# Kernel tuning notes

Measured on AMD Instinct MI355X. Metric: run time of the kernel, lower is better.

## Reference

```python
import jax, jax.numpy as jnp
import numpy as np

EPS = 1e-5


def conv3x3(x, w, b):
    # x [B,C,H,W], w [O,C,3,3], stride 1, pad 1
    y = jax.lax.conv_general_dilated(x, w, (1, 1), ((1, 1), (1, 1)),
                                     dimension_numbers=('NCHW', 'OIHW', 'NCHW'))
    return y + b[None, :, None, None]


def bilinear_gather(x, py, px):
    # x [B,C,H,W]; sampling locations py,px [B,K,H,W] -> [B,C,K,H,W]
    # Zero padding outside the image (matches deform_conv CUDA semantics:
    # out-of-bound corner values contribute 0).
    B, C, H, W = x.shape
    K = py.shape[1]
    x_flat = x.reshape(B, C, H * W)
    y0 = jnp.floor(py)
    x0 = jnp.floor(px)
    out = jnp.zeros((B, C, K, H, W), x.dtype)
    for dy in (0.0, 1.0):
        for dx in (0.0, 1.0):
            yi = y0 + dy
            xi = x0 + dx
            wgt = (1.0 - jnp.abs(py - yi)) * (1.0 - jnp.abs(px - xi))  # [B,K,H,W]
            valid = (yi >= 0) & (yi <= H - 1) & (xi >= 0) & (xi <= W - 1)
            idx = (jnp.clip(yi, 0, H - 1).astype(jnp.int32) * W
                   + jnp.clip(xi, 0, W - 1).astype(jnp.int32)).reshape(B, -1)
            vals = jax.vmap(lambda xf, i: xf[:, i])(x_flat, idx)  # [B,C,K*H*W]
            out = out + (wgt * valid)[:, None] * vals.reshape(B, C, K, H, W)
    return out


def setup_inputs() -> dict:
    key = jax.random.key(0)
    k1, k2, k3 = jax.random.split(key, 3)
    B, C, O, H, W = 4, 64, 64, 128, 128
    x = jax.random.normal(k1, (B, C, H, W), jnp.float32)
    # offset predictor: small init so predicted offsets are modest (realistic)
    off_w = 0.01 * jax.random.normal(k2, (18, C, 3, 3), jnp.float32)
    off_b = jnp.zeros((18,), jnp.float32)
    dc_w = jax.random.normal(k3, (O, C, 3, 3), jnp.float32) / np.sqrt(C * 9)
    dc_b = jnp.zeros((O,), jnp.float32)
    gamma = jnp.ones((O,), jnp.float32)
    beta = jnp.zeros((O,), jnp.float32)
    return {"x": x, "off_w": off_w, "off_b": off_b, "dc_w": dc_w,
            "dc_b": dc_b, "gamma": gamma, "beta": beta}


def reference(x, off_w, off_b, dc_w, dc_b, gamma, beta):
    B, C, H, W = x.shape
    O = dc_w.shape[0]
    K = 9  # 3x3 kernel
    offset = conv3x3(x, off_w, off_b)              # [B,18,H,W]
    off = offset.reshape(B, K, 2, H, W)            # (dy,dx) per kernel tap, row-major
    dyo, dxo = off[:, :, 0], off[:, :, 1]          # [B,K,H,W]
    k = (jnp.arange(3) - 1).astype(x.dtype)        # kernel taps {-1,0,1}
    kgy = jnp.repeat(k, 3)                         # [9] row-major y offsets
    kgx = jnp.tile(k, 3)                           # [9] row-major x offsets
    hh = jnp.arange(H, dtype=x.dtype)
    ww = jnp.arange(W, dtype=x.dtype)
    # stride 1, pad 1: base point = out_pos - 1 + tap; pad is folded into kgy/kgx
    py = hh[None, None, :, None] + kgy[None, :, None, None] + dyo
    px = ww[None, None, None, :] + kgx[None, :, None, None] + dxo
    sampled = bilinear_gather(x, py, px)           # [B,C,K,H,W]
    y = jnp.einsum('ock,bckhw->bohw', dc_w.reshape(O, C, K), sampled)
    y = y + dc_b[None, :, None, None]
    # BatchNorm2d (training mode: biased batch statistics)
    mu = y.mean(axis=(0, 2, 3), keepdims=True)
    var = y.var(axis=(0, 2, 3), keepdims=True)
    yn = (y - mu) * jax.lax.rsqrt(var + EPS)
    return jax.nn.relu(yn * gamma[None, :, None, None] + beta[None, :, None, None])
```

## Files before the change

### kernel.cpp

```cpp
#include <hip/hip_runtime.h>

#define HH 128
#define WW 128
#define HWSZ (HH * WW)
#define CC 64
#define OO 64
#define BB 4
#define NOFF 18
#define KK 576

#define WS_BG     0
#define WS_BGO    18432
#define WS_YBUF   27776
#define WS_PART   2125952

typedef __attribute__((ext_vector_type(8))) short short8;
typedef __attribute__((ext_vector_type(4))) int int4v;
typedef __attribute__((ext_vector_type(2))) unsigned int uint2v;
typedef __attribute__((ext_vector_type(4))) float f32x4;

__device__ inline unsigned bf16rne(float f) {
  unsigned u = __float_as_uint(f);
  u += 0x7fff + ((u >> 16) & 1);
  return u >> 16;
}

__device__ inline float bf16lo(unsigned u) { return __uint_as_float(u << 16); }
__device__ inline float bf16hi(unsigned u) { return __uint_as_float(u & 0xffff0000u); }

__global__ __launch_bounds__(256) void prep_kernel(
    const float* __restrict__ x, const float* __restrict__ off_w,
    const float* __restrict__ dc_w, unsigned int* __restrict__ xTu,
    int* __restrict__ Bg, int* __restrict__ Bgo) {
  int bid = blockIdx.x;
  if (bid < BB * HH * 2) {
    __shared__ float T[CC][64 + 1];
    int b = bid >> 8, rem = bid & 255;
    int h = rem >> 1, wh = (rem & 1) * 64;
    const float* xp = x + (size_t)b * CC * HWSZ + h * WW + wh;
    int j = threadIdx.x;
#pragma unroll
    for (int i = 0; i < 4; ++i) {
      int l = i * 256 + j;
      int c = l >> 4, w4 = l & 15;
      float4 v = *(const float4*)(xp + (size_t)c * HWSZ + w4 * 4);
      T[c][w4 * 4 + 0] = v.x;
      T[c][w4 * 4 + 1] = v.y;
      T[c][w4 * 4 + 2] = v.z;
      T[c][w4 * 4 + 3] = v.w;
    }
    __syncthreads();
    int c2 = threadIdx.x & 31, wq = threadIdx.x >> 5;
    unsigned int* op = xTu + ((size_t)(b * HH + h) * WW + wh) * 32;
#pragma unroll 8
    for (int i = 0; i < 8; ++i) {
      int w = i * 8 + wq;
      unsigned pk = bf16rne(T[2 * c2][w]) | (bf16rne(T[2 * c2 + 1][w]) << 16);
      op[w * 32 + c2] = pk;
    }
  } else {
    int pb = bid - BB * HH * 2;
    int tid = pb * 256 + threadIdx.x;
    int stride = 64 * 256;
    for (int i = tid; i < 72 * 64 * 4; i += stride) {
      int j = i & 3, o = (i >> 2) & 63, g = i >> 8;
      int k2 = g * 4 + j, t = k2 >> 5, jj = k2 & 31;
      unsigned lo = bf16rne(dc_w[o * KK + (2 * jj) * 9 + t]);
      unsigned hi = bf16rne(dc_w[o * KK + (2 * jj + 1) * 9 + t]);
      Bg[i] = (int)(lo | (hi << 16));
    }
    for (int i = tid; i < 72 * 32 * 4; i += stride) {
      int j = i & 3, o = (i >> 2) & 31, g = i >> 7;
      int k2 = g * 4 + j, t = k2 >> 5, jj = k2 & 31;
      unsigned pk = 0;
      if (o < NOFF) {
        unsigned lo = bf16rne(off_w[o * KK + (2 * jj) * 9 + t]);
        unsigned hi = bf16rne(off_w[o * KK + (2 * jj + 1) * 9 + t]);
        pk = lo | (hi << 16);
      }
      Bgo[i] = (int)pk;
    }
  }
}

#define G_ISSUE(i, T, PH)                                                     \
  int4v m##i, da##i, db##i, dcv##i, dd##i;                                    \
  {                                                                           \
    m##i = *(const int4v*)&Mw[(((PH) * 8 + p8) * 9 + (T)) * 4];               \
    unsigned x_ = (unsigned)m##i.x, y_ = (unsigned)m##i.y;                    \
    da##i  = *(const int4v*)&xbu[(x_ & 0xffffu) * 32 + cq4];                  \
    db##i  = *(const int4v*)&xbu[(x_ >> 16) * 32 + cq4];                      \
    dcv##i = *(const int4v*)&xbu[(y_ & 0xffffu) * 32 + cq4];                  \
    dd##i  = *(const int4v*)&xbu[(y_ >> 16) * 32 + cq4];                      \
  }

#define G_BLEND(i, T, PH)                                                     \
  {                                                                           \
    float w00_ = __uint_as_float(((unsigned)m##i.z) << 16);                   \
    float w01_ = __uint_as_float(((unsigned)m##i.z) & 0xffff0000u);           \
    float w10_ = __uint_as_float(((unsigned)m##i.w) << 16);                   \
    float w11_ = __uint_as_float(((unsigned)m##i.w) & 0xffff0000u);           \
    int4v pk_;                                                                \
    _Pragma("unroll")                                                         \
    for (int j = 0; j < 4; ++j) {                                             \
      float slo_ = w00_ * __uint_as_float(((unsigned)da##i[j]) << 16);        \
      slo_ = fmaf(w01_, __uint_as_float(((unsigned)db##i[j]) << 16), slo_);   \
      slo_ = fmaf(w10_, __uint_as_float(((unsigned)dcv##i[j]) << 16), slo_);  \
      slo_ = fmaf(w11_, __uint_as_float(((unsigned)dd##i[j]) << 16), slo_);   \
      float shi_ = w00_ * __uint_as_float(((unsigned)da##i[j]) & 0xffff0000u);\
      shi_ = fmaf(w01_, __uint_as_float(((unsigned)db##i[j]) & 0xffff0000u), shi_);\
      shi_ = fmaf(w10_, __uint_as_float(((unsigned)dcv##i[j]) & 0xffff0000u), shi_);\
      shi_ = fmaf(w11_, __uint_as_float(((unsigned)dd##i[j]) & 0xffff0000u), shi_);\
      pk_[j] = (int)__builtin_amdgcn_perm(__float_as_uint(shi_) + 0x8000u,    \
                                          __float_as_uint(slo_) + 0x8000u,    \
                                          0x07060302u);                       \
    }                                                                         \
    *(int4v*)&A[abase + ((T) & 1) * 544 + ((PH) * 8 + p8) * 34 + cq4] = pk_;  \
  }

#define MFMA_TAP(T)                                                           \
  {                                                                           \
    _Pragma("unroll")                                                         \
    for (int kk2 = 0; kk2 < 2; ++kk2) {                                       \
      int4v av = *(const int4v*)&A[abase + ((T) & 1) * 544 + n16 * 34 + kk2 * 16 + q * 4]; \
      short8 af = __builtin_bit_cast(short8, av);                             \
      int g = (T) * 8 + kk2 * 4 + q;                                          \
      _Pragma("unroll")                                                       \
      for (int nt = 0; nt < 4; ++nt) {                                        \
        int4v bv = *(const int4v*)&Bg[(g * 64 + nt * 16 + n16) * 4];          \
        short8 bfr = __builtin_bit_cast(short8, bv);                          \
        acc[nt] = __builtin_amdgcn_mfma_f32_16x16x32_bf16(af, bfr, acc[nt], 0, 0, 0); \
      }                                                                       \
    }                                                                         \
  }

__global__ __launch_bounds__(256, 6) void fused_kernel(
    const unsigned int* __restrict__ xTu, const int* __restrict__ Bg,
    const int* __restrict__ Bgo, const float* __restrict__ off_b,
    const float* __restrict__ dc_b, unsigned int* __restrict__ ybuf,
    float* __restrict__ part) {
  __shared__ __align__(16) int A[4 * 1088];
  __shared__ __align__(16) int M[4 * 144 * 4];

  int cg = threadIdx.x >> 6, lane = threadIdx.x & 63;
  int wg = (int)blockIdx.x;
  int swz = (wg & 7) * 128 + (wg >> 3);
  int b = swz >> 8, rem = swz & 255;
  int h = rem >> 1, w0 = (rem & 1) * 64;
  int hw0 = h * WW + w0;
  int p0 = cg * 16;
  int abase = cg * 1088;
  int n16 = lane & 15, q = lane >> 4;
  int pg = lane >> 3, part8 = lane & 7;
  const unsigned int* xbu = xTu + (size_t)b * HWSZ * 32;

  f32x4 acc2[2] = {f32x4{0, 0, 0, 0}, f32x4{0, 0, 0, 0}};
#pragma unroll
  for (int t = 0; t < 9; ++t) {
    int ky = t / 3 - 1, kx = t % 3 - 1;
    int cy = h + ky;
    bool vy = (cy >= 0) && (cy < HH);
    int cys = min(max(cy, 0), HH - 1);
    int tb = abase + (t & 1) * 544;
#pragma unroll
    for (int i = 0; i < 2; ++i) {
      int px = i * 8 + pg;
      int cx = w0 + p0 + px + kx;
      bool v = vy && (cx >= 0) && (cx < WW);
      int cxs = min(max(cx, 0), WW - 1);
      int4v val = *(const int4v*)&xbu[(cys * WW + cxs) * 32 + part8 * 4];
      if (!v) { val.x = 0; val.y = 0; val.z = 0; val.w = 0; }
      *(int4v*)&A[tb + px * 34 + part8 * 4] = val;
    }
#pragma unroll
    for (int kk2 = 0; kk2 < 2; ++kk2) {
      int4v av = *(const int4v*)&A[tb + n16 * 34 + kk2 * 16 + q * 4];
      short8 af = __builtin_bit_cast(short8, av);
      int g = t * 8 + kk2 * 4 + q;
#pragma unroll
      for (int nt = 0; nt < 2; ++nt) {
        int4v bv = *(const int4v*)&Bgo[(g * 32 + nt * 16 + n16) * 4];
        short8 bfr = __builtin_bit_cast(short8, bv);
        acc2[nt] = __builtin_amdgcn_mfma_f32_16x16x32_bf16(af, bfr, acc2[nt], 0, 0, 0);
      }
    }
  }
  float* offLw = (float*)&A[abase];
#pragma unroll
  for (int nt = 0; nt < 2; ++nt) {
    int o = nt * 16 + n16;
    if (o < NOFF) {
      float bv = off_b[o];
#pragma unroll
      for (int r = 0; r < 4; ++r) offLw[o * 16 + q * 4 + r] = acc2[nt][r] + bv;
    }
  }

  int* Mw = M + cg * 144 * 4;
#pragma unroll
  for (int it = 0; it < 3; ++it) {
    int m = it * 64 + lane;
    if (m < 144) {
      int pxl = (unsigned)m / 9u;
      int t = m - pxl * 9;
      float dy = offLw[(2 * t) * 16 + pxl];
      float dx = offLw[(2 * t + 1) * 16 + pxl];
      float py = (float)(h + t / 3 - 1) + dy;
      float pxf = (float)(w0 + p0 + pxl + (t % 3) - 1) + dx;
      float fy0 = floorf(py), fx0 = floorf(pxf);
      float ay = py - fy0, ax = pxf - fx0;
      int iy0 = (int)fy0, ix0 = (int)fx0;
      int iy1 = iy0 + 1, ix1 = ix0 + 1;
      float wy0 = 1.0f - ay, wy1 = ay, wx0 = 1.0f - ax, wx1 = ax;
      if (!(iy0 >= 0 && iy0 < HH)) wy0 = 0.0f;
      if (!(iy1 >= 0 && iy1 < HH)) wy1 = 0.0f;
      if (!(ix0 >= 0 && ix0 < WW)) wx0 = 0.0f;
      if (!(ix1 >= 0 && ix1 < WW)) wx1 = 0.0f;
      int cy0 = min(max(iy0, 0), HH - 1), cy1 = min(max(iy1, 0), HH - 1);
      int cx0 = min(max(ix0, 0), WW - 1), cx1 = min(max(ix1, 0), WW - 1);
      int4v mv;
      mv.x = (cy0 * WW + cx0) | ((cy0 * WW + cx1) << 16);
      mv.y = (cy1 * WW + cx0) | ((cy1 * WW + cx1) << 16);
      mv.z = (int)(bf16rne(wy0 * wx0) | (bf16rne(wy0 * wx1) << 16));
      mv.w = (int)(bf16rne(wy1 * wx0) | (bf16rne(wy1 * wx1) << 16));
      *(int4v*)&Mw[m * 4] = mv;
    }
  }

  int p8 = lane >> 3;
  int cq4 = (lane & 7) * 4;
  f32x4 acc[4] = {f32x4{0,0,0,0}, f32x4{0,0,0,0}, f32x4{0,0,0,0}, f32x4{0,0,0,0}};
  G_ISSUE(0, 0, 0)   G_ISSUE(1, 0, 1)
  G_ISSUE(2, 1, 0)   G_ISSUE(3, 1, 1)   G_BLEND(0, 0, 0)   G_BLEND(1, 0, 1)   MFMA_TAP(0)
  G_ISSUE(4, 2, 0)   G_ISSUE(5, 2, 1)   G_BLEND(2, 1, 0)   G_BLEND(3, 1, 1)   MFMA_TAP(1)
  G_ISSUE(6, 3, 0)   G_ISSUE(7, 3, 1)   G_BLEND(4, 2, 0)   G_BLEND(5, 2, 1)   MFMA_TAP(2)
  G_ISSUE(8, 4, 0)   G_ISSUE(9, 4, 1)   G_BLEND(6, 3, 0)   G_BLEND(7, 3, 1)   MFMA_TAP(3)
  G_ISSUE(10, 5, 0)  G_ISSUE(11, 5, 1)  G_BLEND(8, 4, 0)   G_BLEND(9, 4, 1)   MFMA_TAP(4)
  G_ISSUE(12, 6, 0)  G_ISSUE(13, 6, 1)  G_BLEND(10, 5, 0)  G_BLEND(11, 5, 1)  MFMA_TAP(5)
  G_ISSUE(14, 7, 0)  G_ISSUE(15, 7, 1)  G_BLEND(12, 6, 0)  G_BLEND(13, 6, 1)  MFMA_TAP(6)
  G_ISSUE(16, 8, 0)  G_ISSUE(17, 8, 1)  G_BLEND(14, 7, 0)  G_BLEND(15, 7, 1)  MFMA_TAP(7)
  G_BLEND(16, 8, 0)  G_BLEND(17, 8, 1)  MFMA_TAP(8)

  float* SW = (float*)&A[abase];
#pragma unroll
  for (int nt = 0; nt < 4; ++nt) {
    int o = nt * 16 + n16;
    float bv = dc_b[o];
    f32x4 r;
    float s = 0.0f, ss = 0.0f;
#pragma unroll
    for (int r0 = 0; r0 < 4; ++r0) {
      r[r0] = acc[nt][r0] + bv;
      s += r[r0];
      ss += r[r0] * r[r0];
    }
    unsigned pk0 = __builtin_amdgcn_perm(__float_as_uint(r[1]) + 0x8000u,
                                         __float_as_uint(r[0]) + 0x8000u,
                                         0x07060302u);
    unsigned pk1 = __builtin_amdgcn_perm(__float_as_uint(r[3]) + 0x8000u,
                                         __float_as_uint(r[2]) + 0x8000u,
                                         0x07060302u);
    uint2v pk; pk.x = pk0; pk.y = pk1;
    *(uint2v*)&ybuf[(size_t)(b * OO + o) * (HWSZ / 2) + ((hw0 + p0) >> 1) + q * 2] = pk;
    s += __shfl_xor(s, 16);  s += __shfl_xor(s, 32);
    ss += __shfl_xor(ss, 16); ss += __shfl_xor(ss, 32);
    if (lane < 16) {
      SW[nt * 16 + lane] = s;
      SW[64 + nt * 16 + lane] = ss;
    }
  }
  __syncthreads();
  if (threadIdx.x < 64) {
    float ts = 0.0f, tq = 0.0f;
#pragma unroll
    for (int wv = 0; wv < 4; ++wv) {
      const float* Sv = (const float*)&A[wv * 1088];
      ts += Sv[threadIdx.x];
      tq += Sv[64 + threadIdx.x];
    }
    part[(size_t)threadIdx.x * 1024 + blockIdx.x] = ts;
    part[(size_t)(64 + threadIdx.x) * 1024 + blockIdx.x] = tq;
  }
}

__global__ __launch_bounds__(256) void norm_kernel(
    const unsigned int* __restrict__ ybuf, const float* __restrict__ part,
    const float* __restrict__ gamma, const float* __restrict__ beta,
    float* __restrict__ out) {
  __shared__ float red[16];
  int gid = blockIdx.x * 256 + threadIdx.x;
  int o = (blockIdx.x >> 3) & 63;
  float4 v4 = ((const float4*)(part + (size_t)o * 1024))[threadIdx.x];
  float4 w4 = ((const float4*)(part + (size_t)(64 + o) * 1024))[threadIdx.x];
  float s = v4.x + v4.y + v4.z + v4.w;
  float sq = w4.x + w4.y + w4.z + w4.w;
#pragma unroll
  for (int off = 1; off < 64; off <<= 1) {
    s += __shfl_xor(s, off);
    sq += __shfl_xor(sq, off);
  }
  if ((threadIdx.x & 63) == 0) {
    int w = threadIdx.x >> 6;
    red[w] = s;
    red[8 + w] = sq;
  }
  __syncthreads();
  float sm = red[0] + red[1] + red[2] + red[3];
  float sqq = red[8] + red[9] + red[10] + red[11];

  const float invN = 1.0f / (float)(BB * HWSZ);
  float mean = sm * invN;
  float var = sqq * invN - mean * mean;
  float rstd = rsqrtf(var + 1e-5f);
  float g = gamma[o] * rstd;
  float bta = beta[o] - mean * g;
  int4v v = ((const int4v*)ybuf)[gid];
  float4 r0, r1;
  r0.x = fmaxf(bf16lo((unsigned)v.x) * g + bta, 0.0f);
  r0.y = fmaxf(bf16hi((unsigned)v.x) * g + bta, 0.0f);
  r0.z = fmaxf(bf16lo((unsigned)v.y) * g + bta, 0.0f);
  r0.w = fmaxf(bf16hi((unsigned)v.y) * g + bta, 0.0f);
  r1.x = fmaxf(bf16lo((unsigned)v.z) * g + bta, 0.0f);
  r1.y = fmaxf(bf16hi((unsigned)v.z) * g + bta, 0.0f);
  r1.z = fmaxf(bf16lo((unsigned)v.w) * g + bta, 0.0f);
  r1.w = fmaxf(bf16hi((unsigned)v.w) * g + bta, 0.0f);
  ((float4*)out)[gid * 2] = r0;
  ((float4*)out)[gid * 2 + 1] = r1;
}

extern "C" void kernel_launch(void* const* d_in, const int* in_sizes, int n_in,
                              void* d_out, int out_size, void* d_ws, size_t ws_size,
                              hipStream_t stream) {
  const float* x     = (const float*)d_in[0];
  const float* off_w = (const float*)d_in[1];
  const float* off_b = (const float*)d_in[2];
  const float* dc_w  = (const float*)d_in[3];
  const float* dc_b  = (const float*)d_in[4];
  const float* gamma = (const float*)d_in[5];
  const float* beta  = (const float*)d_in[6];
  float* ws = (float*)d_ws;
  int*   Bg     = (int*)(ws + WS_BG);
  int*   Bgo    = (int*)(ws + WS_BGO);
  unsigned int* ybuf = (unsigned int*)(ws + WS_YBUF);
  float* part   = ws + WS_PART;
  float* out = (float*)d_out;
  unsigned int* xTu = (unsigned int*)d_out;

  prep_kernel<<<BB * HH * 2 + 64, 256, 0, stream>>>(x, off_w, dc_w, xTu, Bg, Bgo);
  fused_kernel<<<BB * HWSZ / 64, 256, 0, stream>>>(xTu, Bg, Bgo, off_b, dc_b, ybuf, part);
  norm_kernel<<<BB * OO * HWSZ / (8 * 256), 256, 0, stream>>>(ybuf, part, gamma, beta, out);
}
```

Before: 120.6 us.

## Split deformable-conv taps across wave pairs and double the block grid

Each block now covers 32 pixels instead of 64, so the grid doubles to 2048 blocks. Waves are paired per 16-pixel tile: one wave gathers and runs MFMA for the even taps, the other for the odd taps. The partial accumulators are summed through LDS before the bias, the bf16 store and the BN partial statistics. This shortens each wave's serial gather-blend-MFMA chain and adds parallelism, and occupancy is raised to 7. The cost is an extra LDS exchange and barrier, duplicated offset-conv work within each wave pair, and twice as many BN partials for norm_kernel to read.

```diff
diff --git a/kernel.cpp b/kernel.cpp
--- a/kernel.cpp
+++ b/kernel.cpp
@@ -8,6 +8,7 @@
 #define BB 4
 #define NOFF 18
 #define KK 576
+#define NBLK 2048
 
 #define WS_BG     0
 #define WS_BGO    18432
@@ -83,10 +84,10 @@
   }
 }
 
-#define G_ISSUE(i, T, PH)                                                     \
+#define G_ISSUE(i, K, PH)                                                     \
   int4v m##i, da##i, db##i, dcv##i, dd##i;                                    \
   {                                                                           \
-    m##i = *(const int4v*)&Mw[(((PH) * 8 + p8) * 9 + (T)) * 4];               \
+    m##i = *(const int4v*)&Mw[(((PH) * 8 + p8) * 5 + (K)) * 4];               \
     unsigned x_ = (unsigned)m##i.x, y_ = (unsigned)m##i.y;                    \
     da##i  = *(const int4v*)&xbu[(x_ & 0xffffu) * 32 + cq4];                  \
     db##i  = *(const int4v*)&xbu[(x_ >> 16) * 32 + cq4];                      \
@@ -94,7 +95,7 @@
     dd##i  = *(const int4v*)&xbu[(y_ >> 16) * 32 + cq4];                      \
   }
 
-#define G_BLEND(i, T, PH)                                                     \
+#define G_BLEND(i, K, PH)                                                     \
   {                                                                           \
     float w00_ = __uint_as_float(((unsigned)m##i.z) << 16);                   \
     float w01_ = __uint_as_float(((unsigned)m##i.z) & 0xffff0000u);           \
@@ -115,14 +116,14 @@
                                           __float_as_uint(slo_) + 0x8000u,    \
                                           0x07060302u);                       \
     }                                                                         \
-    *(int4v*)&A[abase + ((T) & 1) * 544 + ((PH) * 8 + p8) * 34 + cq4] = pk_;  \
-  }
-
-#define MFMA_TAP(T)                                                           \
+    *(int4v*)&A[abase + ((K) & 1) * 544 + ((PH) * 8 + p8) * 34 + cq4] = pk_;  \
+  }
+
+#define MFMA_TAP(T, KB)                                                       \
   {                                                                           \
     _Pragma("unroll")                                                         \
     for (int kk2 = 0; kk2 < 2; ++kk2) {                                       \
-      int4v av = *(const int4v*)&A[abase + ((T) & 1) * 544 + n16 * 34 + kk2 * 16 + q * 4]; \
+      int4v av = *(const int4v*)&A[abase + ((KB) & 1) * 544 + n16 * 34 + kk2 * 16 + q * 4]; \
       short8 af = __builtin_bit_cast(short8, av);                             \
       int g = (T) * 8 + kk2 * 4 + q;                                          \
       _Pragma("unroll")                                                       \
@@ -134,22 +135,23 @@
     }                                                                         \
   }
 
-__global__ __launch_bounds__(256, 6) void fused_kernel(
+__global__ __launch_bounds__(256, 7) void fused_kernel(
     const unsigned int* __restrict__ xTu, const int* __restrict__ Bg,
     const int* __restrict__ Bgo, const float* __restrict__ off_b,
     const float* __restrict__ dc_b, unsigned int* __restrict__ ybuf,
     float* __restrict__ part) {
   __shared__ __align__(16) int A[4 * 1088];
-  __shared__ __align__(16) int M[4 * 144 * 4];
-
-  int cg = threadIdx.x >> 6, lane = threadIdx.x & 63;
+  __shared__ __align__(16) int M[4 * 320];
+
+  int cw = threadIdx.x >> 6, lane = threadIdx.x & 63;
+  int tile = cw >> 1, par = cw & 1;
   int wg = (int)blockIdx.x;
-  int swz = (wg & 7) * 128 + (wg >> 3);
-  int b = swz >> 8, rem = swz & 255;
-  int h = rem >> 1, w0 = (rem & 1) * 64;
+  int swz = (wg & 7) * 256 + (wg >> 3);
+  int b = swz >> 9, rem = swz & 511;
+  int h = rem >> 2, w0 = (rem & 3) * 32;
   int hw0 = h * WW + w0;
-  int p0 = cg * 16;
-  int abase = cg * 1088;
+  int p0 = tile * 16;
+  int abase = cw * 1088;
   int n16 = lane & 15, q = lane >> 4;
   int pg = lane >> 3, part8 = lane & 7;
   const unsigned int* xbu = xTu + (size_t)b * HWSZ * 32;
@@ -196,13 +198,15 @@
     }
   }
 
-  int* Mw = M + cg * 144 * 4;
-#pragma unroll
-  for (int it = 0; it < 3; ++it) {
+  int* Mw = M + cw * 320;
+  int nent = par ? 64 : 80;
+#pragma unroll
+  for (int it = 0; it < 2; ++it) {
     int m = it * 64 + lane;
-    if (m < 144) {
-      int pxl = (unsigned)m / 9u;
-      int t = m - pxl * 9;
+    if (m < nent) {
+      int pxl, k, t;
+      if (par) { pxl = m >> 2; k = m & 3; t = 2 * k + 1; }
+      else     { pxl = (int)((unsigned)m / 5u); k = m - pxl * 5; t = 2 * k; }
       float dy = offLw[(2 * t) * 16 + pxl];
       float dx = offLw[(2 * t + 1) * 16 + pxl];
       float py = (float)(h + t / 3 - 1) + dy;
@@ -223,63 +227,76 @@
       mv.y = (cy1 * WW + cx0) | ((cy1 * WW + cx1) << 16);
       mv.z = (int)(bf16rne(wy0 * wx0) | (bf16rne(wy0 * wx1) << 16));
       mv.w = (int)(bf16rne(wy1 * wx0) | (bf16rne(wy1 * wx1) << 16));
-      *(int4v*)&Mw[m * 4] = mv;
+      *(int4v*)&Mw[(pxl * 5 + k) * 4] = mv;
     }
   }
 
   int p8 = lane >> 3;
   int cq4 = (lane & 7) * 4;
   f32x4 acc[4] = {f32x4{0,0,0,0}, f32x4{0,0,0,0}, f32x4{0,0,0,0}, f32x4{0,0,0,0}};
-  G_ISSUE(0, 0, 0)   G_ISSUE(1, 0, 1)
-  G_ISSUE(2, 1, 0)   G_ISSUE(3, 1, 1)   G_BLEND(0, 0, 0)   G_BLEND(1, 0, 1)   MFMA_TAP(0)
-  G_ISSUE(4, 2, 0)   G_ISSUE(5, 2, 1)   G_BLEND(2, 1, 0)   G_BLEND(3, 1, 1)   MFMA_TAP(1)
-  G_ISSUE(6, 3, 0)   G_ISSUE(7, 3, 1)   G_BLEND(4, 2, 0)   G_BLEND(5, 2, 1)   MFMA_TAP(2)
-  G_ISSUE(8, 4, 0)   G_ISSUE(9, 4, 1)   G_BLEND(6, 3, 0)   G_BLEND(7, 3, 1)   MFMA_TAP(3)
-  G_ISSUE(10, 5, 0)  G_ISSUE(11, 5, 1)  G_BLEND(8, 4, 0)   G_BLEND(9, 4, 1)   MFMA_TAP(4)
-  G_ISSUE(12, 6, 0)  G_ISSUE(13, 6, 1)  G_BLEND(10, 5, 0)  G_BLEND(11, 5, 1)  MFMA_TAP(5)
-  G_ISSUE(14, 7, 0)  G_ISSUE(15, 7, 1)  G_BLEND(12, 6, 0)  G_BLEND(13, 6, 1)  MFMA_TAP(6)
-  G_ISSUE(16, 8, 0)  G_ISSUE(17, 8, 1)  G_BLEND(14, 7, 0)  G_BLEND(15, 7, 1)  MFMA_TAP(7)
-  G_BLEND(16, 8, 0)  G_BLEND(17, 8, 1)  MFMA_TAP(8)
-
-  float* SW = (float*)&A[abase];
-#pragma unroll
-  for (int nt = 0; nt < 4; ++nt) {
-    int o = nt * 16 + n16;
-    float bv = dc_b[o];
-    f32x4 r;
-    float s = 0.0f, ss = 0.0f;
-#pragma unroll
-    for (int r0 = 0; r0 < 4; ++r0) {
-      r[r0] = acc[nt][r0] + bv;
-      s += r[r0];
-      ss += r[r0] * r[r0];
-    }
-    unsigned pk0 = __builtin_amdgcn_perm(__float_as_uint(r[1]) + 0x8000u,
-                                         __float_as_uint(r[0]) + 0x8000u,
-                                         0x07060302u);
-    unsigned pk1 = __builtin_amdgcn_perm(__float_as_uint(r[3]) + 0x8000u,
-                                         __float_as_uint(r[2]) + 0x8000u,
-                                         0x07060302u);
-    uint2v pk; pk.x = pk0; pk.y = pk1;
-    *(uint2v*)&ybuf[(size_t)(b * OO + o) * (HWSZ / 2) + ((hw0 + p0) >> 1) + q * 2] = pk;
-    s += __shfl_xor(s, 16);  s += __shfl_xor(s, 32);
-    ss += __shfl_xor(ss, 16); ss += __shfl_xor(ss, 32);
-    if (lane < 16) {
-      SW[nt * 16 + lane] = s;
-      SW[64 + nt * 16 + lane] = ss;
+  if (par == 0) {
+    G_ISSUE(0, 0, 0)  G_ISSUE(1, 0, 1)
+    G_ISSUE(2, 1, 0)  G_ISSUE(3, 1, 1)  G_BLEND(0, 0, 0)  G_BLEND(1, 0, 1)  MFMA_TAP(0, 0)
+    G_ISSUE(4, 2, 0)  G_ISSUE(5, 2, 1)  G_BLEND(2, 1, 0)  G_BLEND(3, 1, 1)  MFMA_TAP(2, 1)
+    G_ISSUE(6, 3, 0)  G_ISSUE(7, 3, 1)  G_BLEND(4, 2, 0)  G_BLEND(5, 2, 1)  MFMA_TAP(4, 2)
+    G_ISSUE(8, 4, 0)  G_ISSUE(9, 4, 1)  G_BLEND(6, 3, 0)  G_BLEND(7, 3, 1)  MFMA_TAP(6, 3)
+    G_BLEND(8, 4, 0)  G_BLEND(9, 4, 1)  MFMA_TAP(8, 4)
+  } else {
+    G_ISSUE(0, 0, 0)  G_ISSUE(1, 0, 1)
+    G_ISSUE(2, 1, 0)  G_ISSUE(3, 1, 1)  G_BLEND(0, 0, 0)  G_BLEND(1, 0, 1)  MFMA_TAP(1, 0)
+    G_ISSUE(4, 2, 0)  G_ISSUE(5, 2, 1)  G_BLEND(2, 1, 0)  G_BLEND(3, 1, 1)  MFMA_TAP(3, 1)
+    G_ISSUE(6, 3, 0)  G_ISSUE(7, 3, 1)  G_BLEND(4, 2, 0)  G_BLEND(5, 2, 1)  MFMA_TAP(5, 2)
+    G_BLEND(6, 3, 0)  G_BLEND(7, 3, 1)  MFMA_TAP(7, 3)
+  }
+
+  if (par) {
+    float* X = (float*)&A[abase];
+#pragma unroll
+    for (int nt = 0; nt < 4; ++nt)
+      *(f32x4*)&X[lane * 16 + nt * 4] = acc[nt];
+  }
+  __syncthreads();
+
+  if (par == 0) {
+    const float* X = (const float*)&A[(cw + 1) * 1088];
+    float* SW = (float*)&A[abase];
+#pragma unroll
+    for (int nt = 0; nt < 4; ++nt) {
+      f32x4 pv = *(const f32x4*)&X[lane * 16 + nt * 4];
+      int o = nt * 16 + n16;
+      float bv = dc_b[o];
+      f32x4 r;
+      float s = 0.0f, ss = 0.0f;
+#pragma unroll
+      for (int r0 = 0; r0 < 4; ++r0) {
+        r[r0] = acc[nt][r0] + pv[r0] + bv;
+        s += r[r0];
+        ss += r[r0] * r[r0];
+      }
+      unsigned pk0 = __builtin_amdgcn_perm(__float_as_uint(r[1]) + 0x8000u,
+                                           __float_as_uint(r[0]) + 0x8000u,
+                                           0x07060302u);
+      unsigned pk1 = __builtin_amdgcn_perm(__float_as_uint(r[3]) + 0x8000u,
+                                           __float_as_uint(r[2]) + 0x8000u,
+                                           0x07060302u);
+      uint2v pk; pk.x = pk0; pk.y = pk1;
+      *(uint2v*)&ybuf[(size_t)(b * OO + o) * (HWSZ / 2) + ((hw0 + p0) >> 1) + q * 2] = pk;
+      s += __shfl_xor(s, 16);  s += __shfl_xor(s, 32);
+      ss += __shfl_xor(ss, 16); ss += __shfl_xor(ss, 32);
+      if (lane < 16) {
+        SW[nt * 16 + lane] = s;
+        SW[64 + nt * 16 + lane] = ss;
+      }
     }
   }
   __syncthreads();
   if (threadIdx.x < 64) {
-    float ts = 0.0f, tq = 0.0f;
-#pragma unroll
-    for (int wv = 0; wv < 4; ++wv) {
-      const float* Sv = (const float*)&A[wv * 1088];
-      ts += Sv[threadIdx.x];
-      tq += Sv[64 + threadIdx.x];
-    }
-    part[(size_t)threadIdx.x * 1024 + blockIdx.x] = ts;
-    part[(size_t)(64 + threadIdx.x) * 1024 + blockIdx.x] = tq;
+    const float* S0 = (const float*)&A[0];
+    const float* S2 = (const float*)&A[2 * 1088];
+    float ts = S0[threadIdx.x] + S2[threadIdx.x];
+    float tq = S0[64 + threadIdx.x] + S2[64 + threadIdx.x];
+    part[(size_t)threadIdx.x * NBLK + blockIdx.x] = ts;
+    part[(size_t)(64 + threadIdx.x) * NBLK + blockIdx.x] = tq;
   }
 }
 
@@ -290,10 +307,12 @@
   __shared__ float red[16];
   int gid = blockIdx.x * 256 + threadIdx.x;
   int o = (blockIdx.x >> 3) & 63;
-  float4 v4 = ((const float4*)(part + (size_t)o * 1024))[threadIdx.x];
-  float4 w4 = ((const float4*)(part + (size_t)(64 + o) * 1024))[threadIdx.x];
-  float s = v4.x + v4.y + v4.z + v4.w;
-  float sq = w4.x + w4.y + w4.z + w4.w;
+  const float4* p4 = (const float4*)(part + (size_t)o * NBLK);
+  const float4* q4 = (const float4*)(part + (size_t)(64 + o) * NBLK);
+  float4 a0 = p4[threadIdx.x], a1 = p4[threadIdx.x + 256];
+  float4 b0 = q4[threadIdx.x], b1 = q4[threadIdx.x + 256];
+  float s = (a0.x + a0.y + a0.z + a0.w) + (a1.x + a1.y + a1.z + a1.w);
+  float sq = (b0.x + b0.y + b0.z + b0.w) + (b1.x + b1.y + b1.z + b1.w);
 #pragma unroll
   for (int off = 1; off < 64; off <<= 1) {
     s += __shfl_xor(s, off);
@@ -347,6 +366,6 @@
   unsigned int* xTu = (unsigned int*)d_out;
 
   prep_kernel<<<BB * HH * 2 + 64, 256, 0, stream>>>(x, off_w, dc_w, xTu, Bg, Bgo);
-  fused_kernel<<<BB * HWSZ / 64, 256, 0, stream>>>(xTu, Bg, Bgo, off_b, dc_b, ybuf, part);
+  fused_kernel<<<NBLK, 256, 0, stream>>>(xTu, Bg, Bgo, off_b, dc_b, ybuf, part);
   norm_kernel<<<BB * OO * HWSZ / (8 * 256), 256, 0, stream>>>(ybuf, part, gamma, beta, out);
 }
```

Result: slower. 183.2 us (+51.9%).
